# Optimization experiments

Measured on AMD Instinct MI355X. Metric: run time of the kernel, lower is better.

Reference implementation:

```python
import jax, jax.numpy as jnp
import numpy as np
import math

N_FREQS = 32
MARGIN = 0.1
CHOUT = 270
POS_DIM = 2 * N_FREQS ** 2  # 2048


def fourier_emb(positions):
    # positions: [..., 2] in [0, 1]
    width = 1.0 + 2.0 * MARGIN
    p = (positions + MARGIN) / width
    f = jnp.arange(N_FREQS, dtype=p.dtype)
    two_pi = 2.0 * math.pi
    # phase[..., i, j] = 2*pi*(x*i + y*j)  -> flatten to [..., F*F]
    phase = two_pi * (p[..., 0][..., None, None] * f[:, None]
                      + p[..., 1][..., None, None] * f[None, :])
    phase = phase.reshape(*phase.shape[:-2], N_FREQS * N_FREQS)
    return jnp.concatenate([jnp.sin(phase), jnp.cos(phase)], axis=-1)  # [..., 2F^2]


def setup_inputs() -> dict:
    key = jax.random.key(0)
    k1, k2, k3 = jax.random.split(key, 3)
    B, C, T = 32, 273, 3000
    brain_data = jax.random.normal(k1, (B, C, T), dtype=jnp.float32)
    channel_layout = jax.random.uniform(k2, (B, C, 2), dtype=jnp.float32)
    heads = jax.random.normal(k3, (CHOUT, POS_DIM), dtype=jnp.float32) / POS_DIM ** 0.5
    return {"brain_data": brain_data, "channel_layout": channel_layout, "heads": heads}


def reference(brain_data, channel_layout, heads):
    # Eval mode: all channels valid, no dropout mask, zero score offset.
    emb = fourier_emb(channel_layout)                      # [B, C, D]
    scores = jnp.einsum('bcd,od->boc', emb, heads)         # [B, O, C]
    weights = jax.nn.softmax(scores, axis=-1)              # softmax over channels
    out = jnp.einsum('bct,boc->bot', brain_data, weights)  # [B, O, T]
    return out
```

## Files before the change

### kernel.cpp

```cpp
#include <hip/hip_runtime.h>
#include <hip/hip_bf16.h>
#include <hip/hip_fp16.h>

#define NB 32
#define NC 273
#define NT 3000
#define NO 270
#define ND 2048
#define CP 288

typedef _Float16 f16x8 __attribute__((ext_vector_type(8)));
typedef float f32x4 __attribute__((ext_vector_type(4)));

#define S_OFF 55296000UL
#define W_OFF 64730880UL
#define H_OFF 69707520UL

__device__ __forceinline__ unsigned short f2h_bits(float f) {
  _Float16 h = (_Float16)f;
  unsigned short u;
  __builtin_memcpy(&u, &h, 2);
  return u;
}

__global__ void heads_cvt_kernel(const float* __restrict__ heads,
                                 _Float16* __restrict__ hh) {
  const size_t idx = ((size_t)blockIdx.x * 256 + threadIdx.x) * 8;
  const float4 a = *reinterpret_cast<const float4*>(heads + idx);
  const float4 c = *reinterpret_cast<const float4*>(heads + idx + 4);
  f16x8 v;
  v[0] = (_Float16)a.x; v[1] = (_Float16)a.y; v[2] = (_Float16)a.z; v[3] = (_Float16)a.w;
  v[4] = (_Float16)c.x; v[5] = (_Float16)c.y; v[6] = (_Float16)c.z; v[7] = (_Float16)c.w;
  *reinterpret_cast<f16x8*>(hh + idx) = v;
}

__global__ void scores_kernel(const _Float16* __restrict__ hh,
                              const float* __restrict__ layout,
                              float* __restrict__ scores) {
  __shared__ _Float16 As[64][72];
  __shared__ _Float16 Bs[64][72];
  const int gid = blockIdx.x;
  const int tid = threadIdx.x;
  const int b = gid / 25;
  const int rem = gid % 25;
  const int o0 = (rem / 5) * 64;
  const int c0 = (rem % 5) * 64;
  const int lane = tid & 63, w = tid >> 6;
  const int wm = (w >> 1) * 32, wn = (w & 1) * 32;
  const int ln = lane & 15, quad = lane >> 4;
  const int sr = tid >> 2;
  const int sk = (tid & 3) * 16;

  const int ch = c0 + sr;
  float px = 0.f, py = 0.f;
  if (ch < NC) {
    const float inv = 1.0f / 1.2f;
    const float* lp = layout + ((size_t)b * NC + ch) * 2;
    px = (lp[0] + 0.1f) * inv;
    py = (lp[1] + 0.1f) * inv;
  }

  f32x4 acc[2][2] = {};

  for (int k0 = 0; k0 < ND; k0 += 64) {
    {
      const int o = o0 + sr;
      uint4 u0 = {0, 0, 0, 0}, u1 = {0, 0, 0, 0};
      if (o < NO) {
        const uint4* p = reinterpret_cast<const uint4*>(hh + (size_t)o * ND + k0 + sk);
        u0 = p[0]; u1 = p[1];
      }
      *reinterpret_cast<uint4*>(&As[sr][sk]) = u0;
      *reinterpret_cast<uint4*>(&As[sr][sk + 8]) = u1;
    }
    {
      const int kg = k0 + sk;
      const int dd = kg & 1023;
      const float base = px * (float)(dd >> 5) + py * (float)(dd & 31)
                       + ((kg < 1024) ? 0.0f : 0.25f);
      f16x8 h0, h1;
#pragma unroll
      for (int s = 0; s < 8; ++s) {
        float ph = base + py * (float)s;
        ph -= floorf(ph);
        h0[s] = (_Float16)__builtin_amdgcn_sinf(ph);
      }
#pragma unroll
      for (int s = 0; s < 8; ++s) {
        float ph = base + py * (float)(s + 8);
        ph -= floorf(ph);
        h1[s] = (_Float16)__builtin_amdgcn_sinf(ph);
      }
      *reinterpret_cast<f16x8*>(&Bs[sr][sk]) = h0;
      *reinterpret_cast<f16x8*>(&Bs[sr][sk + 8]) = h1;
    }
    __syncthreads();
#pragma unroll
    for (int ks = 0; ks < 64; ks += 32) {
      const int kf = ks + quad * 8;
      const f16x8 a0 = *reinterpret_cast<const f16x8*>(&As[wm + ln][kf]);
      const f16x8 a1 = *reinterpret_cast<const f16x8*>(&As[wm + 16 + ln][kf]);
      const f16x8 b0 = *reinterpret_cast<const f16x8*>(&Bs[wn + ln][kf]);
      const f16x8 b1 = *reinterpret_cast<const f16x8*>(&Bs[wn + 16 + ln][kf]);
      acc[0][0] = __builtin_amdgcn_mfma_f32_16x16x32_f16(a0, b0, acc[0][0], 0, 0, 0);
      acc[0][1] = __builtin_amdgcn_mfma_f32_16x16x32_f16(a0, b1, acc[0][1], 0, 0, 0);
      acc[1][0] = __builtin_amdgcn_mfma_f32_16x16x32_f16(a1, b0, acc[1][0], 0, 0, 0);
      acc[1][1] = __builtin_amdgcn_mfma_f32_16x16x32_f16(a1, b1, acc[1][1], 0, 0, 0);
    }
    __syncthreads();
  }

  float* sB = scores + (size_t)b * NO * NC;
#pragma unroll
  for (int i = 0; i < 2; ++i) {
    const int ob = o0 + wm + 16 * i + quad * 4;
#pragma unroll
    for (int j = 0; j < 2; ++j) {
      const int cc = c0 + wn + 16 * j + ln;
      if (cc >= NC) continue;
#pragma unroll
      for (int r = 0; r < 4; ++r) {
        const int o = ob + r;
        if (o < NO) sB[(size_t)o * NC + cc] = acc[i][j][r];
      }
    }
  }
}

__global__ void softmax_kernel(const float* __restrict__ sc,
                               _Float16* __restrict__ wq) {
  const int row = blockIdx.x * 4 + (threadIdx.x >> 6);
  const int lane = threadIdx.x & 63;
  const float* p = sc + (size_t)row * NC;
  _Float16* q = wq + (size_t)row * CP;
  float v[5];
  float m = -3.0e38f;
#pragma unroll
  for (int k = 0; k < 5; ++k) {
    const int c = lane + k * 64;
    v[k] = (c < NC) ? p[c] : -3.0e38f;
    m = fmaxf(m, v[k]);
  }
#pragma unroll
  for (int off = 32; off > 0; off >>= 1) m = fmaxf(m, __shfl_xor(m, off));
  float s = 0.f;
#pragma unroll
  for (int k = 0; k < 5; ++k) {
    v[k] = expf(v[k] - m);
    s += v[k];
  }
#pragma unroll
  for (int off = 32; off > 0; off >>= 1) s += __shfl_xor(s, off);
  const float r = 1.0f / s;
#pragma unroll
  for (int k = 0; k < 5; ++k) {
    const int c = lane + k * 64;
    if (c < NC) q[c] = (_Float16)(v[k] * r);
    else if (c < CP) q[c] = (_Float16)0.f;
  }
}

#define TS 64

__global__ __launch_bounds__(256) void out_kernel(
    const _Float16* __restrict__ wq,
    const float* __restrict__ brain,
    float* __restrict__ out) {
  __shared__ _Float16 Bs[TS][296];
  __shared__ float tile[32][68];
  const int b = blockIdx.y;
  const int t0 = blockIdx.x * TS;
  const int tid = threadIdx.x;
  const int lane = tid & 63, w = tid >> 6;
  const int om = (w >> 1) * 32, tn = (w & 1) * 32;
  const int ln = lane & 15, quad = lane >> 4;

  const int cl = tid >> 3;
  const int tq = (tid & 7) * 4;
  const int tt = tid & 63;
  const int cg = tid >> 6;
  for (int p = 0; p < 9; ++p) {
    const int c = p * 32 + cl;
    float4 v0 = {0.f, 0.f, 0.f, 0.f}, v1 = v0;
    if (c < NC) {
      const float* src = brain + ((size_t)b * NC + c) * NT + t0 + tq;
      const int tb = t0 + tq;
      if (tb + 35 < NT) {
        v0 = *reinterpret_cast<const float4*>(src);
        v1 = *reinterpret_cast<const float4*>(src + 32);
      } else {
        if (tb + 0 < NT) v0.x = src[0];
        if (tb + 1 < NT) v0.y = src[1];
        if (tb + 2 < NT) v0.z = src[2];
        if (tb + 3 < NT) v0.w = src[3];
        if (tb + 32 < NT) v1.x = src[32];
        if (tb + 33 < NT) v1.y = src[33];
        if (tb + 34 < NT) v1.z = src[34];
        if (tb + 35 < NT) v1.w = src[35];
      }
    }
    *reinterpret_cast<float4*>(&tile[cl][tq]) = v0;
    *reinterpret_cast<float4*>(&tile[cl][tq + 32]) = v1;
    __syncthreads();
    {
      unsigned short h[8];
#pragma unroll
      for (int s = 0; s < 8; ++s) h[s] = f2h_bits(tile[cg * 8 + s][tt]);
      uint4 u;
      u.x = (unsigned)h[0] | ((unsigned)h[1] << 16);
      u.y = (unsigned)h[2] | ((unsigned)h[3] << 16);
      u.z = (unsigned)h[4] | ((unsigned)h[5] << 16);
      u.w = (unsigned)h[6] | ((unsigned)h[7] << 16);
      *reinterpret_cast<uint4*>(&Bs[tt][p * 32 + cg * 8]) = u;
    }
    __syncthreads();
  }

  const _Float16* Wb = wq + (size_t)b * NO * CP;
  float* oB = out + (size_t)b * NO * NT;
  const int tA = tn + ln;
  const int tB = tn + 16 + ln;

  for (int ot = 0; ot < 5; ++ot) {
    const int o0 = ot * 64;
    int ra = o0 + om + ln;      if (ra > NO - 1) ra = NO - 1;
    int rb = o0 + om + 16 + ln; if (rb > NO - 1) rb = NO - 1;
    const _Float16* pA0 = Wb + (size_t)ra * CP + quad * 8;
    const _Float16* pA1 = Wb + (size_t)rb * CP + quad * 8;

    f32x4 acc[2][2] = {};
#pragma unroll
    for (int s = 0; s < 9; ++s) {
      const int kf = s * 32;
      const f16x8 a0 = *reinterpret_cast<const f16x8*>(pA0 + kf);
      const f16x8 a1 = *reinterpret_cast<const f16x8*>(pA1 + kf);
      const f16x8 b0 = *reinterpret_cast<const f16x8*>(&Bs[tA][kf + quad * 8]);
      const f16x8 b1 = *reinterpret_cast<const f16x8*>(&Bs[tB][kf + quad * 8]);
      acc[0][0] = __builtin_amdgcn_mfma_f32_16x16x32_f16(a0, b0, acc[0][0], 0, 0, 0);
      acc[0][1] = __builtin_amdgcn_mfma_f32_16x16x32_f16(a0, b1, acc[0][1], 0, 0, 0);
      acc[1][0] = __builtin_amdgcn_mfma_f32_16x16x32_f16(a1, b0, acc[1][0], 0, 0, 0);
      acc[1][1] = __builtin_amdgcn_mfma_f32_16x16x32_f16(a1, b1, acc[1][1], 0, 0, 0);
    }

#pragma unroll
    for (int i = 0; i < 2; ++i) {
      const int ob = o0 + om + 16 * i + quad * 4;
#pragma unroll
      for (int j = 0; j < 2; ++j) {
        const int t = t0 + tn + 16 * j + ln;
        if (t >= NT) continue;
#pragma unroll
        for (int r = 0; r < 4; ++r) {
          const int o = ob + r;
          if (o < NO) oB[(size_t)o * NT + t] = acc[i][j][r];
        }
      }
    }
  }
}

extern "C" void kernel_launch(void* const* d_in, const int* in_sizes, int n_in,
                              void* d_out, int out_size, void* d_ws, size_t ws_size,
                              hipStream_t stream) {
  const float* brain = (const float*)d_in[0];
  const float* layout = (const float*)d_in[1];
  const float* heads = (const float*)d_in[2];
  for (int i = 0; i < n_in; ++i) {
    if (in_sizes[i] == NB * NC * NT) brain = (const float*)d_in[i];
    else if (in_sizes[i] == NB * NC * 2) layout = (const float*)d_in[i];
    else if (in_sizes[i] == NO * ND) heads = (const float*)d_in[i];
  }
  float* out = (float*)d_out;

  float* scores = (float*)((char*)d_ws + S_OFF);
  _Float16* wq = (_Float16*)((char*)d_ws + W_OFF);
  _Float16* hh = (_Float16*)((char*)d_ws + H_OFF);

  heads_cvt_kernel<<<NO, 256, 0, stream>>>(heads, hh);
  scores_kernel<<<800, 256, 0, stream>>>(hh, layout, scores);
  softmax_kernel<<<(NB * NO) / 4, 256, 0, stream>>>(scores, wq);
  out_kernel<<<dim3(47, NB), 256, 0, stream>>>(wq, brain, out);
}
```

Before: 282.3 us.

## Software-pipeline brain tile loads and prefetch weight fragments into registers

The staging loop now issues the global loads for the next 32-channel chunk before converting the current one. The barriers become raw s_barrier calls guarded by an LDS-only waitcnt, so the outstanding global loads are not forced to drain at each barrier. The weight A-fragments for the first output tile are loaded before staging and the next tile's fragments are prefetched after each tile's MFMAs, so the output loop no longer waits on those global reads. This adds 72 VGPRs of fragment state plus the next-chunk prefetch registers, which may lower occupancy or cause spills.

```diff
diff --git a/kernel.cpp b/kernel.cpp
--- a/kernel.cpp
+++ b/kernel.cpp
@@ -162,6 +162,20 @@
 
 #define TS 64
 
+__device__ __forceinline__ void load_a_frags(const _Float16* __restrict__ Wb,
+                                             int o0, int om, int ln, int quad,
+                                             f16x8* a0f, f16x8* a1f) {
+  int ra = o0 + om + ln;      if (ra > NO - 1) ra = NO - 1;
+  int rb = o0 + om + 16 + ln; if (rb > NO - 1) rb = NO - 1;
+  const _Float16* pA0 = Wb + (size_t)ra * CP + quad * 8;
+  const _Float16* pA1 = Wb + (size_t)rb * CP + quad * 8;
+#pragma unroll
+  for (int s = 0; s < 9; ++s) {
+    a0f[s] = *reinterpret_cast<const f16x8*>(pA0 + s * 32);
+    a1f[s] = *reinterpret_cast<const f16x8*>(pA1 + s * 32);
+  }
+}
+
 __global__ __launch_bounds__(256) void out_kernel(
     const _Float16* __restrict__ wq,
     const float* __restrict__ brain,
@@ -175,16 +189,22 @@
   const int om = (w >> 1) * 32, tn = (w & 1) * 32;
   const int ln = lane & 15, quad = lane >> 4;
 
+  const _Float16* Wb = wq + (size_t)b * NO * CP;
+
+  f16x8 a0f[9], a1f[9];
+  load_a_frags(Wb, 0, om, ln, quad, a0f, a1f);
+
   const int cl = tid >> 3;
   const int tq = (tid & 7) * 4;
   const int tt = tid & 63;
   const int cg = tid >> 6;
-  for (int p = 0; p < 9; ++p) {
-    const int c = p * 32 + cl;
-    float4 v0 = {0.f, 0.f, 0.f, 0.f}, v1 = v0;
+
+  const int tb = t0 + tq;
+  float4 v0 = {0.f, 0.f, 0.f, 0.f}, v1 = v0;
+  {
+    const int c = cl;
     if (c < NC) {
-      const float* src = brain + ((size_t)b * NC + c) * NT + t0 + tq;
-      const int tb = t0 + tq;
+      const float* src = brain + ((size_t)b * NC + c) * NT + tb;
       if (tb + 35 < NT) {
         v0 = *reinterpret_cast<const float4*>(src);
         v1 = *reinterpret_cast<const float4*>(src + 32);
@@ -199,9 +219,34 @@
         if (tb + 35 < NT) v1.w = src[35];
       }
     }
+  }
+
+  for (int p = 0; p < 9; ++p) {
     *reinterpret_cast<float4*>(&tile[cl][tq]) = v0;
     *reinterpret_cast<float4*>(&tile[cl][tq + 32]) = v1;
-    __syncthreads();
+    float4 n0 = {0.f, 0.f, 0.f, 0.f}, n1 = n0;
+    if (p < 8) {
+      const int c = (p + 1) * 32 + cl;
+      if (c < NC) {
+        const float* src = brain + ((size_t)b * NC + c) * NT + tb;
+        if (tb + 35 < NT) {
+          n0 = *reinterpret_cast<const float4*>(src);
+          n1 = *reinterpret_cast<const float4*>(src + 32);
+        } else {
+          if (tb + 0 < NT) n0.x = src[0];
+          if (tb + 1 < NT) n0.y = src[1];
+          if (tb + 2 < NT) n0.z = src[2];
+          if (tb + 3 < NT) n0.w = src[3];
+          if (tb + 32 < NT) n1.x = src[32];
+          if (tb + 33 < NT) n1.y = src[33];
+          if (tb + 34 < NT) n1.z = src[34];
+          if (tb + 35 < NT) n1.w = src[35];
+        }
+      }
+    }
+    asm volatile("s_waitcnt lgkmcnt(0)" ::: "memory");
+    __builtin_amdgcn_sched_barrier(0);
+    __builtin_amdgcn_s_barrier();
     {
       unsigned short h[8];
 #pragma unroll
@@ -213,34 +258,32 @@
       u.w = (unsigned)h[6] | ((unsigned)h[7] << 16);
       *reinterpret_cast<uint4*>(&Bs[tt][p * 32 + cg * 8]) = u;
     }
-    __syncthreads();
-  }
-
-  const _Float16* Wb = wq + (size_t)b * NO * CP;
+    asm volatile("s_waitcnt lgkmcnt(0)" ::: "memory");
+    __builtin_amdgcn_sched_barrier(0);
+    __builtin_amdgcn_s_barrier();
+    v0 = n0; v1 = n1;
+  }
+
   float* oB = out + (size_t)b * NO * NT;
   const int tA = tn + ln;
   const int tB = tn + 16 + ln;
 
+#pragma unroll
   for (int ot = 0; ot < 5; ++ot) {
     const int o0 = ot * 64;
-    int ra = o0 + om + ln;      if (ra > NO - 1) ra = NO - 1;
-    int rb = o0 + om + 16 + ln; if (rb > NO - 1) rb = NO - 1;
-    const _Float16* pA0 = Wb + (size_t)ra * CP + quad * 8;
-    const _Float16* pA1 = Wb + (size_t)rb * CP + quad * 8;
-
     f32x4 acc[2][2] = {};
 #pragma unroll
     for (int s = 0; s < 9; ++s) {
       const int kf = s * 32;
-      const f16x8 a0 = *reinterpret_cast<const f16x8*>(pA0 + kf);
-      const f16x8 a1 = *reinterpret_cast<const f16x8*>(pA1 + kf);
       const f16x8 b0 = *reinterpret_cast<const f16x8*>(&Bs[tA][kf + quad * 8]);
       const f16x8 b1 = *reinterpret_cast<const f16x8*>(&Bs[tB][kf + quad * 8]);
-      acc[0][0] = __builtin_amdgcn_mfma_f32_16x16x32_f16(a0, b0, acc[0][0], 0, 0, 0);
-      acc[0][1] = __builtin_amdgcn_mfma_f32_16x16x32_f16(a0, b1, acc[0][1], 0, 0, 0);
-      acc[1][0] = __builtin_amdgcn_mfma_f32_16x16x32_f16(a1, b0, acc[1][0], 0, 0, 0);
-      acc[1][1] = __builtin_amdgcn_mfma_f32_16x16x32_f16(a1, b1, acc[1][1], 0, 0, 0);
-    }
+      acc[0][0] = __builtin_amdgcn_mfma_f32_16x16x32_f16(a0f[s], b0, acc[0][0], 0, 0, 0);
+      acc[0][1] = __builtin_amdgcn_mfma_f32_16x16x32_f16(a0f[s], b1, acc[0][1], 0, 0, 0);
+      acc[1][0] = __builtin_amdgcn_mfma_f32_16x16x32_f16(a1f[s], b0, acc[1][0], 0, 0, 0);
+      acc[1][1] = __builtin_amdgcn_mfma_f32_16x16x32_f16(a1f[s], b1, acc[1][1], 0, 0, 0);
+    }
+
+    if (ot < 4) load_a_frags(Wb, o0 + 64, om, ln, quad, a0f, a1f);
 
 #pragma unroll
     for (int i = 0; i < 2; ++i) {
```

Result: no change. 279.5 us (-1.0%).

## Pipeline brain chunk loads with MFMA via double-buffered swizzled raw tile

Applied to the files above, without the earlier changes.

Replaces the two-phase staging (convert all 288 channels into an f16 transposed tile, then loop over output tiles) with a software pipeline over 9 channel chunks. Raw fp32 brain data is double-buffered in XOR-swizzled shared memory, prefetched two chunks ahead in registers, and converted to f16 while building the MFMA B fragments. All 5 output-row tiles are accumulated at once (80 accumulator floats), and weight fragments are loaded one step ahead. Shared memory drops so 2 blocks per CU are requested, but register pressure rises sharply and may cause spills.

```diff
diff --git a/kernel.cpp b/kernel.cpp
--- a/kernel.cpp
+++ b/kernel.cpp
@@ -160,31 +160,36 @@
   }
 }
 
-#define TS 64
-
-__global__ __launch_bounds__(256) void out_kernel(
+__global__ __launch_bounds__(256, 2) void out_kernel(
     const _Float16* __restrict__ wq,
     const float* __restrict__ brain,
     float* __restrict__ out) {
-  __shared__ _Float16 Bs[TS][296];
-  __shared__ float tile[32][68];
+  __shared__ float raw[2][32][68];
   const int b = blockIdx.y;
-  const int t0 = blockIdx.x * TS;
+  const int t0 = blockIdx.x * 64;
   const int tid = threadIdx.x;
   const int lane = tid & 63, w = tid >> 6;
   const int om = (w >> 1) * 32, tn = (w & 1) * 32;
   const int ln = lane & 15, quad = lane >> 4;
 
+  const _Float16* Wb = wq + (size_t)b * NO * CP;
+
   const int cl = tid >> 3;
   const int tq = (tid & 7) * 4;
-  const int tt = tid & 63;
-  const int cg = tid >> 6;
-  for (int p = 0; p < 9; ++p) {
-    const int c = p * 32 + cl;
-    float4 v0 = {0.f, 0.f, 0.f, 0.f}, v1 = v0;
+  const int tb = t0 + tq;
+  const int wsw = (cl >> 3) << 4;
+  const int ws0 = tq ^ wsw;
+  const int ws1 = (tq + 32) ^ wsw;
+
+  const int rc0 = (tn + ln) ^ (quad << 4);
+  const int rc1 = (tn + 16 + ln) ^ (quad << 4);
+
+  auto load_chunk = [&](int ci, float4& v0, float4& v1) {
+    float4 z = {0.f, 0.f, 0.f, 0.f};
+    v0 = z; v1 = z;
+    const int c = ci * 32 + cl;
     if (c < NC) {
-      const float* src = brain + ((size_t)b * NC + c) * NT + t0 + tq;
-      const int tb = t0 + tq;
+      const float* src = brain + ((size_t)b * NC + c) * NT + tb;
       if (tb + 35 < NT) {
         v0 = *reinterpret_cast<const float4*>(src);
         v1 = *reinterpret_cast<const float4*>(src + 32);
@@ -199,52 +204,86 @@
         if (tb + 35 < NT) v1.w = src[35];
       }
     }
-    *reinterpret_cast<float4*>(&tile[cl][tq]) = v0;
-    *reinterpret_cast<float4*>(&tile[cl][tq + 32]) = v1;
-    __syncthreads();
+  };
+
+  auto store_raw = [&](int buf, const float4& v0, const float4& v1) {
+    *reinterpret_cast<float4*>(&raw[buf][cl][ws0]) = v0;
+    *reinterpret_cast<float4*>(&raw[buf][cl][ws1]) = v1;
+  };
+
+  auto load_a = [&](int s, f16x8 (&a)[10]) {
+    const int kcol = s * 32 + quad * 8;
+#pragma unroll
+    for (int ot = 0; ot < 5; ++ot) {
+      int r0 = ot * 64 + om + ln;      if (r0 > NO - 1) r0 = NO - 1;
+      int r1 = ot * 64 + om + 16 + ln; if (r1 > NO - 1) r1 = NO - 1;
+      a[2 * ot]     = *reinterpret_cast<const f16x8*>(Wb + (size_t)r0 * CP + kcol);
+      a[2 * ot + 1] = *reinterpret_cast<const f16x8*>(Wb + (size_t)r1 * CP + kcol);
+    }
+  };
+
+  f32x4 acc[5][2][2] = {};
+
+  auto do_mfma = [&](const f16x8 (&a)[10], f16x8 b0, f16x8 b1) {
+#pragma unroll
+    for (int ot = 0; ot < 5; ++ot) {
+      acc[ot][0][0] = __builtin_amdgcn_mfma_f32_16x16x32_f16(a[2*ot],   b0, acc[ot][0][0], 0, 0, 0);
+      acc[ot][0][1] = __builtin_amdgcn_mfma_f32_16x16x32_f16(a[2*ot],   b1, acc[ot][0][1], 0, 0, 0);
+      acc[ot][1][0] = __builtin_amdgcn_mfma_f32_16x16x32_f16(a[2*ot+1], b0, acc[ot][1][0], 0, 0, 0);
+      acc[ot][1][1] = __builtin_amdgcn_mfma_f32_16x16x32_f16(a[2*ot+1], b1, acc[ot][1][1], 0, 0, 0);
+    }
+  };
+
+  f16x8 aE[10], aO[10];
+  float4 rA0, rA1, rB0, rB1;
+
+  load_chunk(0, rA0, rA1);
+  load_a(0, aE);
+  load_chunk(1, rB0, rB1);
+  store_raw(0, rA0, rA1);
+  load_chunk(2, rA0, rA1);
+  asm volatile("s_waitcnt lgkmcnt(0)" ::: "memory");
+  __builtin_amdgcn_sched_barrier(0);
+  __builtin_amdgcn_s_barrier();
+
+#pragma unroll
+  for (int s = 0; s < 9; ++s) {
+    if (s < 8) {
+      if (((s + 1) & 1) == 0) load_a(s + 1, aE); else load_a(s + 1, aO);
+    }
+    if (s < 8) {
+      if (((s + 1) & 1) == 0) {
+        store_raw(0, rA0, rA1);
+        if (s < 6) load_chunk(s + 3, rA0, rA1);
+      } else {
+        store_raw(1, rB0, rB1);
+        if (s < 6) load_chunk(s + 3, rB0, rB1);
+      }
+    }
+    f16x8 b0, b1;
     {
-      unsigned short h[8];
-#pragma unroll
-      for (int s = 0; s < 8; ++s) h[s] = f2h_bits(tile[cg * 8 + s][tt]);
-      uint4 u;
-      u.x = (unsigned)h[0] | ((unsigned)h[1] << 16);
-      u.y = (unsigned)h[2] | ((unsigned)h[3] << 16);
-      u.z = (unsigned)h[4] | ((unsigned)h[5] << 16);
-      u.w = (unsigned)h[6] | ((unsigned)h[7] << 16);
-      *reinterpret_cast<uint4*>(&Bs[tt][p * 32 + cg * 8]) = u;
-    }
-    __syncthreads();
-  }
-
-  const _Float16* Wb = wq + (size_t)b * NO * CP;
+      const float* rb = &raw[s & 1][0][0];
+#pragma unroll
+      for (int j = 0; j < 8; ++j) {
+        const int row = quad * 8 + j;
+        b0[j] = (_Float16)rb[row * 68 + rc0];
+        b1[j] = (_Float16)rb[row * 68 + rc1];
+      }
+    }
+    if (s < 8) {
+      asm volatile("s_waitcnt lgkmcnt(0)" ::: "memory");
+      __builtin_amdgcn_sched_barrier(0);
+      __builtin_amdgcn_s_barrier();
+    }
+    if ((s & 1) == 0) do_mfma(aE, b0, b1); else do_mfma(aO, b0, b1);
+  }
+
   float* oB = out + (size_t)b * NO * NT;
-  const int tA = tn + ln;
-  const int tB = tn + 16 + ln;
-
+#pragma unroll
   for (int ot = 0; ot < 5; ++ot) {
-    const int o0 = ot * 64;
-    int ra = o0 + om + ln;      if (ra > NO - 1) ra = NO - 1;
-    int rb = o0 + om + 16 + ln; if (rb > NO - 1) rb = NO - 1;
-    const _Float16* pA0 = Wb + (size_t)ra * CP + quad * 8;
-    const _Float16* pA1 = Wb + (size_t)rb * CP + quad * 8;
-
-    f32x4 acc[2][2] = {};
-#pragma unroll
-    for (int s = 0; s < 9; ++s) {
-      const int kf = s * 32;
-      const f16x8 a0 = *reinterpret_cast<const f16x8*>(pA0 + kf);
-      const f16x8 a1 = *reinterpret_cast<const f16x8*>(pA1 + kf);
-      const f16x8 b0 = *reinterpret_cast<const f16x8*>(&Bs[tA][kf + quad * 8]);
-      const f16x8 b1 = *reinterpret_cast<const f16x8*>(&Bs[tB][kf + quad * 8]);
-      acc[0][0] = __builtin_amdgcn_mfma_f32_16x16x32_f16(a0, b0, acc[0][0], 0, 0, 0);
-      acc[0][1] = __builtin_amdgcn_mfma_f32_16x16x32_f16(a0, b1, acc[0][1], 0, 0, 0);
-      acc[1][0] = __builtin_amdgcn_mfma_f32_16x16x32_f16(a1, b0, acc[1][0], 0, 0, 0);
-      acc[1][1] = __builtin_amdgcn_mfma_f32_16x16x32_f16(a1, b1, acc[1][1], 0, 0, 0);
-    }
-
 #pragma unroll
     for (int i = 0; i < 2; ++i) {
-      const int ob = o0 + om + 16 * i + quad * 4;
+      const int ob = ot * 64 + om + 16 * i + quad * 4;
 #pragma unroll
       for (int j = 0; j < 2; ++j) {
         const int t = t0 + tn + 16 * j + ln;
@@ -252,7 +291,7 @@
 #pragma unroll
         for (int r = 0; r < 4; ++r) {
           const int o = ob + r;
-          if (o < NO) oB[(size_t)o * NT + t] = acc[i][j][r];
+          if (o < NO) oB[(size_t)o * NT + t] = acc[ot][i][j][r];
         }
       }
     }
```

Result: slower. 290.4 us (+2.9%).
